# Optimization experiments

Hardware: AMD Instinct MI355X
Metric: run time of the kernel (lower is better)

The kernel has to match this reference:

```python
import jax, jax.numpy as jnp
import numpy as np

N, DEG, D_IN, D_HID = 50000, 16, 963, 256


def setup_inputs() -> dict:
    key = jax.random.key(0)
    ks = jax.random.split(key, 8)
    s = 0.02
    neighbours = jax.random.randint(ks[0], (N, DEG), 0, N)
    shape_features = jax.random.normal(ks[1], (N, D_IN), dtype=jnp.float32)
    # layer 0: D_IN -> D_HID; layers 1..13 (stacked): D_HID -> D_HID; extra: D_HID -> 3
    W_self0 = jax.random.normal(ks[2], (D_IN, D_HID), dtype=jnp.float32) * s
    W_neigh0 = jax.random.normal(ks[3], (D_IN, D_HID), dtype=jnp.float32) * s
    b0 = jnp.zeros((D_HID,), jnp.float32)
    W_self = jax.random.normal(ks[4], (13, D_HID, D_HID), dtype=jnp.float32) * s
    W_neigh = jax.random.normal(ks[5], (13, D_HID, D_HID), dtype=jnp.float32) * s
    b = jnp.zeros((13, D_HID), jnp.float32)
    W_extra = jax.random.normal(ks[6], (D_HID, 3), dtype=jnp.float32) * s
    b_extra = jnp.zeros((3,), jnp.float32)
    return {
        "neighbours": neighbours,
        "shape_features": shape_features,
        "W_self0": W_self0, "W_neigh0": W_neigh0, "b0": b0,
        "W_self": W_self, "W_neigh": W_neigh, "b": b,
        "W_extra": W_extra, "b_extra": b_extra,
    }


def _gcn(x, neighbours, Ws, Wn, bias):
    # gather neighbour features [N, DEG, D] and sum-aggregate, plus self transform
    agg = jnp.take(x, neighbours, axis=0).sum(axis=1)
    return x @ Ws + agg @ Wn + bias


def reference(neighbours, shape_features, W_self0, W_neigh0, b0, W_self, W_neigh, b, W_extra, b_extra):
    x = jax.nn.relu(_gcn(shape_features, neighbours, W_self0, W_neigh0, b0))
    for i in range(6):  # 6 residual blocks of 2 GCN layers each
        temp = x
        x = jax.nn.relu(_gcn(x, neighbours, W_self[2 * i], W_neigh[2 * i], b[2 * i]))
        x = jax.nn.relu(_gcn(x, neighbours, W_self[2 * i + 1], W_neigh[2 * i + 1], b[2 * i + 1]))
        x = (temp + x) / 2
    x = jax.nn.relu(_gcn(x, neighbours, W_self[12], W_neigh[12], b[12]))
    coordinates = x @ W_extra + b_extra  # extra layer called without neighbours -> linear
    return (x, coordinates)
```

## Files before the change

kernel.cpp:

```cpp
#include <hip/hip_runtime.h>
#include <hip/hip_bf16.h>
#include <hip/hip_fp16.h>
#include <stdint.h>

#define NNODES 50000
#define NPAD   50048
#define DEG    16
#define DIN    963
#define K0PAD  992
#define DHID   256
#define SCALE  (1.0f / 1024.0f)
#define ISCALE 1024.0f

typedef __attribute__((ext_vector_type(4))) float    f32x4;
typedef __attribute__((ext_vector_type(8))) _Float16 f16x8;
typedef __attribute__((ext_vector_type(4))) _Float16 f16x4;

typedef const __attribute__((address_space(1))) void GV;
typedef __attribute__((address_space(3))) void LV;

__device__ __forceinline__ void gl2lds16(const void* g, void* l) {
    __builtin_amdgcn_global_load_lds((GV*)g, (LV*)l, 16, 0, 0);
}

__global__ __launch_bounds__(256) void gemm_dual0(
    const _Float16* __restrict__ A, int K,
    const _Float16* __restrict__ Wp,
    _Float16* __restrict__ ys, _Float16* __restrict__ yn)
{
    __shared__ _Float16 lds[2][2][4096];

    const int tid  = threadIdx.x;
    const int w    = tid >> 6;
    const int lane = tid & 63;
    const int bm   = blockIdx.x * 128;
    const int nb   = blockIdx.y * 128;

    const int KT = K >> 5;

    auto stage = [&](int s, int kt) {
        const int k0 = kt << 5;
#pragma unroll
        for (int i = 0; i < 2; ++i) {
            const int j   = w + (i << 2);
            const int c   = (j << 6) + lane;
            const int row = c & 127;
            const int k8  = (c >> 7) << 3;
            gl2lds16(A  + (size_t)(bm + row) * K + k0 + k8, &lds[s][0][(size_t)j << 9]);
            gl2lds16(Wp + (size_t)(nb + row) * K + k0 + k8, &lds[s][1][(size_t)j << 9]);
        }
    };

    const int wm = (w >> 1) << 6;
    const int wn = (w & 1) << 6;
    const int lr = lane & 15;
    const int kh = lane >> 4;

    f32x4 acc[4][4] = {};

    stage(0, 0);
    __syncthreads();
    int cur = 0;
    for (int kt = 0; kt < KT; ++kt) {
        if (kt + 1 < KT) stage(cur ^ 1, kt + 1);
        f16x8 a[4], b[4];
#pragma unroll
        for (int mi = 0; mi < 4; ++mi)
            a[mi] = *(const f16x8*)&lds[cur][0][((kh << 7) + wm + (mi << 4) + lr) << 3];
#pragma unroll
        for (int ni = 0; ni < 4; ++ni)
            b[ni] = *(const f16x8*)&lds[cur][1][((kh << 7) + wn + (ni << 4) + lr) << 3];
#pragma unroll
        for (int mi = 0; mi < 4; ++mi)
#pragma unroll
            for (int ni = 0; ni < 4; ++ni)
                acc[mi][ni] = __builtin_amdgcn_mfma_f32_16x16x32_f16(a[mi], b[ni], acc[mi][ni], 0, 0, 0);
        __syncthreads();
        cur ^= 1;
    }

    _Float16* C = (blockIdx.y < 2) ? ys : yn;
    const int cb = (nb & 255) + wn;
#pragma unroll
    for (int mi = 0; mi < 4; ++mi) {
        const size_t rbase = (size_t)(bm + wm + (mi << 4) + (kh << 2)) << 8;
#pragma unroll
        for (int ni = 0; ni < 4; ++ni) {
            const int col = cb + (ni << 4) + lr;
#pragma unroll
            for (int r = 0; r < 4; ++r)
                C[rbase + ((size_t)r << 8) + col] = (_Float16)acc[mi][ni][r];
        }
    }
}

template<int FINAL>
__global__ __launch_bounds__(512) void fused_layer(
    const _Float16* __restrict__ X, const int* __restrict__ nbr,
    const _Float16* __restrict__ W, const float* __restrict__ bias,
    const _Float16* __restrict__ res,
    _Float16* __restrict__ outh, float* __restrict__ outf)
{
    __shared__ _Float16 ldsA[2][4096];
    __shared__ _Float16 ldsB[2][8192];

    const int tid  = threadIdx.x;
    const int w    = tid >> 6;
    const int lane = tid & 63;
    const int bm   = blockIdx.x << 7;

    const int growg = bm + (tid >> 2);
    const int nrow  = (growg < NNODES) ? growg : (NNODES - 1);
    const int4* np  = (const int4*)(nbr + nrow * DEG);
    const int4 q0 = np[0], q1 = np[1], q2 = np[2], q3 = np[3];
    const int kq = (tid & 3) << 3;

    auto stage = [&](int s, int kt) {
        if (kt < 8) {
            const int c = tid;
            gl2lds16(X + ((size_t)(bm + (c & 127)) << 8) + (kt << 5) + ((c >> 7) << 3),
                     &ldsA[s][(size_t)c << 3]);
        } else {
            const int kl = ((kt & 7) << 5) + kq;
            auto LD = [&](int r) -> f16x8 {
                return *(const f16x8*)(X + ((size_t)r << 8) + kl);
            };
            const f16x8 t0 = (LD(q0.x) + LD(q0.y)) + (LD(q0.z) + LD(q0.w));
            const f16x8 t1 = (LD(q1.x) + LD(q1.y)) + (LD(q1.z) + LD(q1.w));
            const f16x8 t2 = (LD(q2.x) + LD(q2.y)) + (LD(q2.z) + LD(q2.w));
            const f16x8 t3 = (LD(q3.x) + LD(q3.y)) + (LD(q3.z) + LD(q3.w));
            const f16x8 sum = (t0 + t1) + (t2 + t3);
            *(f16x8*)&ldsA[s][(size_t)(((tid & 3) << 7) + (tid >> 2)) << 3] = sum;
        }
#pragma unroll
        for (int i = 0; i < 2; ++i) {
            const int c = (i << 9) + tid;
            gl2lds16(W + ((size_t)(c & 255) << 9) + (kt << 5) + ((c >> 8) << 3),
                     &ldsB[s][(size_t)c << 3]);
        }
    };

    const int wm = (w >> 2) << 6;
    const int wn = (w & 3) << 6;
    const int lr = lane & 15;
    const int kh = lane >> 4;

    f32x4 acc[4][4] = {};

    stage(0, 0);
    __syncthreads();
    int cur = 0;
    for (int kt = 0; kt < 16; ++kt) {
        if (kt + 1 < 16) stage(cur ^ 1, kt + 1);
        f16x8 a[4], b[4];
#pragma unroll
        for (int mi = 0; mi < 4; ++mi)
            a[mi] = *(const f16x8*)&ldsA[cur][((kh << 7) + wm + (mi << 4) + lr) << 3];
#pragma unroll
        for (int ni = 0; ni < 4; ++ni)
            b[ni] = *(const f16x8*)&ldsB[cur][((kh << 8) + wn + (ni << 4) + lr) << 3];
#pragma unroll
        for (int mi = 0; mi < 4; ++mi)
#pragma unroll
            for (int ni = 0; ni < 4; ++ni)
                acc[mi][ni] = __builtin_amdgcn_mfma_f32_16x16x32_f16(a[mi], b[ni], acc[mi][ni], 0, 0, 0);
        __syncthreads();
        cur ^= 1;
    }

    const int r0 = kh << 2;
#pragma unroll
    for (int mi = 0; mi < 4; ++mi) {
        const int grow0 = bm + wm + (mi << 4) + r0;
#pragma unroll
        for (int ni = 0; ni < 4; ++ni) {
            const int col = wn + (ni << 4) + lr;
            const float bcol = bias[col] * SCALE;
#pragma unroll
            for (int r = 0; r < 4; ++r) {
                const int grow = grow0 + r;
                float s = acc[mi][ni][r] + bcol;
                s = fmaxf(s, 0.f);
                if (res) s = ((float)res[((size_t)grow << 8) + col] + s) * 0.5f;
                if (FINAL) {
                    if (grow < NNODES) outf[((size_t)grow << 8) + col] = s * ISCALE;
                } else {
                    outh[((size_t)grow << 8) + col] = (_Float16)s;
                }
            }
        }
    }
}

__global__ __launch_bounds__(256) void combine0(
    const _Float16* __restrict__ ys, const _Float16* __restrict__ yn,
    const int* __restrict__ nbr, const float* __restrict__ bias,
    _Float16* __restrict__ outh)
{
    const int w    = threadIdx.x >> 6;
    const int lane = threadIdx.x & 63;
    const int n    = (blockIdx.x << 2) + w;
    const int c4   = lane << 2;
    const size_t base = ((size_t)n << 8) + c4;

    const f16x4 ysv = *(const f16x4*)(ys + base);
    const float4 bv = *(const float4*)(bias + c4);
    float s0 = (float)ysv[0] + bv.x * SCALE;
    float s1 = (float)ysv[1] + bv.y * SCALE;
    float s2 = (float)ysv[2] + bv.z * SCALE;
    float s3 = (float)ysv[3] + bv.w * SCALE;

    const int* nr = nbr + n * DEG;
#pragma unroll
    for (int j = 0; j < DEG; ++j) {
        const f16x4 v = *(const f16x4*)(yn + (((size_t)nr[j]) << 8) + c4);
        s0 += (float)v[0]; s1 += (float)v[1]; s2 += (float)v[2]; s3 += (float)v[3];
    }
    f16x4 o;
    o[0] = (_Float16)fmaxf(s0, 0.f); o[1] = (_Float16)fmaxf(s1, 0.f);
    o[2] = (_Float16)fmaxf(s2, 0.f); o[3] = (_Float16)fmaxf(s3, 0.f);
    *(f16x4*)(outh + base) = o;
}

__global__ __launch_bounds__(64) void coords_kernel(
    const float* __restrict__ x, const float* __restrict__ We,
    const float* __restrict__ be, float* __restrict__ out3, int N)
{
    const int n = blockIdx.x;
    const int l = threadIdx.x;
    const float4 xv = *(const float4*)(x + (size_t)n * 256 + l * 4);
    float p0 = 0.f, p1 = 0.f, p2 = 0.f;
    const float xs[4] = {xv.x, xv.y, xv.z, xv.w};
#pragma unroll
    for (int i = 0; i < 4; ++i) {
        const int cidx = l * 4 + i;
        p0 += xs[i] * We[cidx * 3 + 0];
        p1 += xs[i] * We[cidx * 3 + 1];
        p2 += xs[i] * We[cidx * 3 + 2];
    }
#pragma unroll
    for (int off = 32; off > 0; off >>= 1) {
        p0 += __shfl_down(p0, off);
        p1 += __shfl_down(p1, off);
        p2 += __shfl_down(p2, off);
    }
    if (l == 0) {
        out3[(size_t)n * 3 + 0] = p0 + be[0];
        out3[(size_t)n * 3 + 1] = p1 + be[1];
        out3[(size_t)n * 3 + 2] = p2 + be[2];
    }
}

__global__ __launch_bounds__(256) void conv_sf(const float* __restrict__ sf,
                                               _Float16* __restrict__ sfb)
{
    const int idx = blockIdx.x * 256 + threadIdx.x;
    const int row = idx / 124;
    const int k8  = (idx % 124) << 3;
    f16x8 o = {};
    if (row < NNODES) {
#pragma unroll
        for (int i = 0; i < 8; ++i) {
            const int k = k8 + i;
            o[i] = (k < DIN) ? (_Float16)(sf[(size_t)row * DIN + k] * SCALE) : (_Float16)0.f;
        }
    }
    *(f16x8*)(sfb + (size_t)row * K0PAD + k8) = o;
}

__global__ __launch_bounds__(256) void pack_w0(const float* __restrict__ Ws0,
                                               const float* __restrict__ Wn0,
                                               _Float16* __restrict__ Wp0)
{
    const int idx = blockIdx.x * 256 + threadIdx.x;
    const int nn  = idx & 511;
    const int k8  = idx >> 9;
    const float* W = (nn < 256) ? Ws0 : Wn0;
    const int n0 = nn & 255;
    f16x8 o;
#pragma unroll
    for (int i = 0; i < 8; ++i) {
        const int k = (k8 << 3) + i;
        o[i] = (k < DIN) ? (_Float16)W[(size_t)k * 256 + n0] : (_Float16)0.f;
    }
    *(f16x8*)(Wp0 + (size_t)nn * K0PAD + (k8 << 3)) = o;
}

__global__ __launch_bounds__(256) void pack_w2(const float* __restrict__ Ws,
                                               const float* __restrict__ Wn,
                                               _Float16* __restrict__ Wpk2)
{
    const int idx = blockIdx.x * 256 + threadIdx.x;
    const int n   = idx & 255;
    const int k8  = (idx >> 8) & 63;
    const int l   = idx >> 14;
    f16x8 o;
#pragma unroll
    for (int i = 0; i < 8; ++i) {
        const int k = (k8 << 3) + i;
        const float* W = (k < 256) ? Ws : Wn;
        o[i] = (_Float16)W[(size_t)l * 65536 + (k & 255) * 256 + n];
    }
    *(f16x8*)(Wpk2 + (size_t)l * 131072 + (size_t)n * 512 + (k8 << 3)) = o;
}

extern "C" void kernel_launch(void* const* d_in, const int* in_sizes, int n_in,
                              void* d_out, int out_size, void* d_ws, size_t ws_size,
                              hipStream_t stream)
{
    const int*   nbr = (const int*)d_in[0];
    const float* sf  = (const float*)d_in[1];
    const float* Ws0 = (const float*)d_in[2];
    const float* Wn0 = (const float*)d_in[3];
    const float* b0  = (const float*)d_in[4];
    const float* Ws  = (const float*)d_in[5];
    const float* Wn  = (const float*)d_in[6];
    const float* bb  = (const float*)d_in[7];
    const float* We  = (const float*)d_in[8];
    const float* be  = (const float*)d_in[9];
    float* out = (float*)d_out;

    uint8_t* w = (uint8_t*)d_ws;
    _Float16* sfb  = (_Float16*)w;
    _Float16* P    = (_Float16*)w;
    _Float16* Q    = P + (size_t)NPAD * 256;
    _Float16* Wpk2 = Q + (size_t)NPAD * 256;
    _Float16* Wp0  = (_Float16*)(w + (size_t)NPAD * K0PAD * 2);
    _Float16* ysb  = Wp0 + (size_t)512 * K0PAD;
    _Float16* ynb  = ysb + (size_t)NPAD * 256;

    conv_sf<<<NPAD * 124 / 256, 256, 0, stream>>>(sf, sfb);
    pack_w0<<<512 * 124 / 256, 256, 0, stream>>>(Ws0, Wn0, Wp0);

    gemm_dual0<<<dim3(NPAD / 128, 4), 256, 0, stream>>>(sfb, K0PAD, Wp0, ysb, ynb);
    pack_w2<<<13 * 64 * 256 / 256, 256, 0, stream>>>(Ws, Wn, Wpk2);
    combine0<<<NNODES / 4, 256, 0, stream>>>(ysb, ynb, nbr, b0, P);

    const int fg = NPAD / 128;

    for (int t = 0; t < 6; ++t) {
        const int lA = 2 * t, lB = lA + 1;
        fused_layer<0><<<fg, 512, 0, stream>>>(P, nbr, Wpk2 + (size_t)lA * 131072,
                                               bb + lA * 256, nullptr, Q, nullptr);
        fused_layer<0><<<fg, 512, 0, stream>>>(Q, nbr, Wpk2 + (size_t)lB * 131072,
                                               bb + lB * 256, P, P, nullptr);
    }

    fused_layer<1><<<fg, 512, 0, stream>>>(P, nbr, Wpk2 + (size_t)12 * 131072,
                                           bb + 12 * 256, nullptr, nullptr, out);

    coords_kernel<<<NNODES, 64, 0, stream>>>(out, We, be, out + (size_t)NNODES * 256, NNODES);
}
```

Before: 1.591 ms.

## Restructure fused GCN layer: 64-row tiles, direct-global MFMA operands, pipelined gather

```diff
diff --git a/kernel.cpp b/kernel.cpp
--- a/kernel.cpp
+++ b/kernel.cpp
@@ -95,83 +95,102 @@
 }
 
 template<int FINAL>
-__global__ __launch_bounds__(512) void fused_layer(
+__global__ __launch_bounds__(256) void fused_layer(
     const _Float16* __restrict__ X, const int* __restrict__ nbr,
     const _Float16* __restrict__ W, const float* __restrict__ bias,
     const _Float16* __restrict__ res,
     _Float16* __restrict__ outh, float* __restrict__ outf)
 {
-    __shared__ _Float16 ldsA[2][4096];
-    __shared__ _Float16 ldsB[2][8192];
+    __shared__ _Float16 ldsG[2][2048];
 
     const int tid  = threadIdx.x;
     const int w    = tid >> 6;
     const int lane = tid & 63;
-    const int bm   = blockIdx.x << 7;
-
-    const int growg = bm + (tid >> 2);
+
+    const int nwg = gridDim.x, bid = blockIdx.x;
+    const int q = nwg >> 3, r_ = nwg & 7, xc = bid & 7;
+    const int wgid = (xc < r_ ? xc * (q + 1) : r_ * (q + 1) + (xc - r_) * q) + (bid >> 3);
+    const int bm = wgid << 6;
+
+    const int growg = bm + lane;
     const int nrow  = (growg < NNODES) ? growg : (NNODES - 1);
     const int4* np  = (const int4*)(nbr + nrow * DEG);
     const int4 q0 = np[0], q1 = np[1], q2 = np[2], q3 = np[3];
-    const int kq = (tid & 3) << 3;
-
-    auto stage = [&](int s, int kt) {
-        if (kt < 8) {
-            const int c = tid;
-            gl2lds16(X + ((size_t)(bm + (c & 127)) << 8) + (kt << 5) + ((c >> 7) << 3),
-                     &ldsA[s][(size_t)c << 3]);
-        } else {
-            const int kl = ((kt & 7) << 5) + kq;
-            auto LD = [&](int r) -> f16x8 {
-                return *(const f16x8*)(X + ((size_t)r << 8) + kl);
-            };
-            const f16x8 t0 = (LD(q0.x) + LD(q0.y)) + (LD(q0.z) + LD(q0.w));
-            const f16x8 t1 = (LD(q1.x) + LD(q1.y)) + (LD(q1.z) + LD(q1.w));
-            const f16x8 t2 = (LD(q2.x) + LD(q2.y)) + (LD(q2.z) + LD(q2.w));
-            const f16x8 t3 = (LD(q3.x) + LD(q3.y)) + (LD(q3.z) + LD(q3.w));
-            const f16x8 sum = (t0 + t1) + (t2 + t3);
-            *(f16x8*)&ldsA[s][(size_t)(((tid & 3) << 7) + (tid >> 2)) << 3] = sum;
-        }
-#pragma unroll
-        for (int i = 0; i < 2; ++i) {
-            const int c = (i << 9) + tid;
-            gl2lds16(W + ((size_t)(c & 255) << 9) + (kt << 5) + ((c >> 8) << 3),
-                     &ldsB[s][(size_t)c << 3]);
-        }
-    };
-
-    const int wm = (w >> 2) << 6;
-    const int wn = (w & 3) << 6;
+    const int kqo = w << 3;
+
+    const int wn = w << 6;
     const int lr = lane & 15;
     const int kh = lane >> 4;
 
     f32x4 acc[4][4] = {};
 
-    stage(0, 0);
-    __syncthreads();
-    int cur = 0;
-    for (int kt = 0; kt < 16; ++kt) {
-        if (kt + 1 < 16) stage(cur ^ 1, kt + 1);
+    auto GLD = [&](int r, int ko) -> f16x8 {
+        return *(const f16x8*)(X + ((size_t)r << 8) + ko);
+    };
+
+    f16x8 g0 = GLD(q0.x, kqo), g1 = GLD(q0.y, kqo), g2 = GLD(q0.z, kqo), g3 = GLD(q0.w, kqo);
+    f16x8 g4 = GLD(q1.x, kqo), g5 = GLD(q1.y, kqo), g6 = GLD(q1.z, kqo), g7 = GLD(q1.w, kqo);
+
+#pragma unroll
+    for (int kt = 0; kt < 8; ++kt) {
         f16x8 a[4], b[4];
 #pragma unroll
         for (int mi = 0; mi < 4; ++mi)
-            a[mi] = *(const f16x8*)&ldsA[cur][((kh << 7) + wm + (mi << 4) + lr) << 3];
+            a[mi] = *(const f16x8*)(X + ((size_t)(bm + (mi << 4) + lr) << 8) + (kt << 5) + (kh << 3));
 #pragma unroll
         for (int ni = 0; ni < 4; ++ni)
-            b[ni] = *(const f16x8*)&ldsB[cur][((kh << 8) + wn + (ni << 4) + lr) << 3];
+            b[ni] = *(const f16x8*)(W + ((size_t)(wn + (ni << 4) + lr) << 9) + (kt << 5) + (kh << 3));
 #pragma unroll
         for (int mi = 0; mi < 4; ++mi)
 #pragma unroll
             for (int ni = 0; ni < 4; ++ni)
                 acc[mi][ni] = __builtin_amdgcn_mfma_f32_16x16x32_f16(a[mi], b[ni], acc[mi][ni], 0, 0, 0);
+    }
+
+    {
+        f16x8 s0 = ((g0 + g1) + (g2 + g3)) + ((g4 + g5) + (g6 + g7));
+        g0 = GLD(q2.x, kqo); g1 = GLD(q2.y, kqo); g2 = GLD(q2.z, kqo); g3 = GLD(q2.w, kqo);
+        g4 = GLD(q3.x, kqo); g5 = GLD(q3.y, kqo); g6 = GLD(q3.z, kqo); g7 = GLD(q3.w, kqo);
+        f16x8 s1 = ((g0 + g1) + (g2 + g3)) + ((g4 + g5) + (g6 + g7));
+        *(f16x8*)&ldsG[0][(w << 9) + (lane << 3)] = s0 + s1;
+    }
+    __syncthreads();
+
+#pragma unroll
+    for (int kt = 8; kt < 16; ++kt) {
+        const int cb = kt & 1;
+        const int ko = ((kt - 7) << 5) + kqo;
+        f16x8 h0, h1, h2, h3, h4, h5, h6, h7;
+        if (kt < 15) {
+            h0 = GLD(q0.x, ko); h1 = GLD(q0.y, ko); h2 = GLD(q0.z, ko); h3 = GLD(q0.w, ko);
+            h4 = GLD(q1.x, ko); h5 = GLD(q1.y, ko); h6 = GLD(q1.z, ko); h7 = GLD(q1.w, ko);
+        }
+        f16x8 a[4], b[4];
+#pragma unroll
+        for (int ni = 0; ni < 4; ++ni)
+            b[ni] = *(const f16x8*)(W + ((size_t)(wn + (ni << 4) + lr) << 9) + (kt << 5) + (kh << 3));
+#pragma unroll
+        for (int mi = 0; mi < 4; ++mi)
+            a[mi] = *(const f16x8*)&ldsG[cb][(kh << 9) + (((mi << 4) + lr) << 3)];
+#pragma unroll
+        for (int mi = 0; mi < 4; ++mi)
+#pragma unroll
+            for (int ni = 0; ni < 4; ++ni)
+                acc[mi][ni] = __builtin_amdgcn_mfma_f32_16x16x32_f16(a[mi], b[ni], acc[mi][ni], 0, 0, 0);
+        if (kt < 15) {
+            f16x8 s0 = ((h0 + h1) + (h2 + h3)) + ((h4 + h5) + (h6 + h7));
+            h0 = GLD(q2.x, ko); h1 = GLD(q2.y, ko); h2 = GLD(q2.z, ko); h3 = GLD(q2.w, ko);
+            h4 = GLD(q3.x, ko); h5 = GLD(q3.y, ko); h6 = GLD(q3.z, ko); h7 = GLD(q3.w, ko);
+            f16x8 s1 = ((h0 + h1) + (h2 + h3)) + ((h4 + h5) + (h6 + h7));
+            *(f16x8*)&ldsG[cb ^ 1][(w << 9) + (lane << 3)] = s0 + s1;
+        }
         __syncthreads();
-        cur ^= 1;
     }
 
     const int r0 = kh << 2;
 #pragma unroll
     for (int mi = 0; mi < 4; ++mi) {
-        const int grow0 = bm + wm + (mi << 4) + r0;
+        const int grow0 = bm + (mi << 4) + r0;
 #pragma unroll
         for (int ni = 0; ni < 4; ++ni) {
             const int col = wn + (ni << 4) + lr;
@@ -336,17 +355,17 @@
     pack_w2<<<13 * 64 * 256 / 256, 256, 0, stream>>>(Ws, Wn, Wpk2);
     combine0<<<NNODES / 4, 256, 0, stream>>>(ysb, ynb, nbr, b0, P);
 
-    const int fg = NPAD / 128;
+    const int fg = NPAD / 64;
 
     for (int t = 0; t < 6; ++t) {
         const int lA = 2 * t, lB = lA + 1;
-        fused_layer<0><<<fg, 512, 0, stream>>>(P, nbr, Wpk2 + (size_t)lA * 131072,
+        fused_layer<0><<<fg, 256, 0, stream>>>(P, nbr, Wpk2 + (size_t)lA * 131072,
                                                bb + lA * 256, nullptr, Q, nullptr);
-        fused_layer<0><<<fg, 512, 0, stream>>>(Q, nbr, Wpk2 + (size_t)lB * 131072,
+        fused_layer<0><<<fg, 256, 0, stream>>>(Q, nbr, Wpk2 + (size_t)lB * 131072,
                                                bb + lB * 256, P, P, nullptr);
     }
 
-    fused_layer<1><<<fg, 512, 0, stream>>>(P, nbr, Wpk2 + (size_t)12 * 131072,
+    fused_layer<1><<<fg, 256, 0, stream>>>(P, nbr, Wpk2 + (size_t)12 * 131072,
                                            bb + 12 * 256, nullptr, nullptr, out);
 
     coords_kernel<<<NNODES, 64, 0, stream>>>(out, We, be, out + (size_t)NNODES * 256, NNODES);
```

After: 2.602 ms. 1.64x slower.

## Split fused gather+GEMM into separate gather kernel and N-tiled GEMM

Applied to the files above, without the earlier changes.

```diff
diff --git a/kernel.cpp b/kernel.cpp
--- a/kernel.cpp
+++ b/kernel.cpp
@@ -95,53 +95,37 @@
 }
 
 template<int FINAL>
-__global__ __launch_bounds__(512) void fused_layer(
-    const _Float16* __restrict__ X, const int* __restrict__ nbr,
-    const _Float16* __restrict__ W, const float* __restrict__ bias,
+__global__ __launch_bounds__(256) void gemm_hidden(
+    const _Float16* __restrict__ X, const _Float16* __restrict__ AG,
+    const _Float16* __restrict__ Wp,
+    const float* __restrict__ bias,
     const _Float16* __restrict__ res,
     _Float16* __restrict__ outh, float* __restrict__ outf)
 {
-    __shared__ _Float16 ldsA[2][4096];
-    __shared__ _Float16 ldsB[2][8192];
+    __shared__ _Float16 lds[2][2][4096];
 
     const int tid  = threadIdx.x;
     const int w    = tid >> 6;
     const int lane = tid & 63;
-    const int bm   = blockIdx.x << 7;
-
-    const int growg = bm + (tid >> 2);
-    const int nrow  = (growg < NNODES) ? growg : (NNODES - 1);
-    const int4* np  = (const int4*)(nbr + nrow * DEG);
-    const int4 q0 = np[0], q1 = np[1], q2 = np[2], q3 = np[3];
-    const int kq = (tid & 3) << 3;
+    const int bm   = blockIdx.x * 128;
+    const int nb   = blockIdx.y << 7;
 
     auto stage = [&](int s, int kt) {
-        if (kt < 8) {
-            const int c = tid;
-            gl2lds16(X + ((size_t)(bm + (c & 127)) << 8) + (kt << 5) + ((c >> 7) << 3),
-                     &ldsA[s][(size_t)c << 3]);
-        } else {
-            const int kl = ((kt & 7) << 5) + kq;
-            auto LD = [&](int r) -> f16x8 {
-                return *(const f16x8*)(X + ((size_t)r << 8) + kl);
-            };
-            const f16x8 t0 = (LD(q0.x) + LD(q0.y)) + (LD(q0.z) + LD(q0.w));
-            const f16x8 t1 = (LD(q1.x) + LD(q1.y)) + (LD(q1.z) + LD(q1.w));
-            const f16x8 t2 = (LD(q2.x) + LD(q2.y)) + (LD(q2.z) + LD(q2.w));
-            const f16x8 t3 = (LD(q3.x) + LD(q3.y)) + (LD(q3.z) + LD(q3.w));
-            const f16x8 sum = (t0 + t1) + (t2 + t3);
-            *(f16x8*)&ldsA[s][(size_t)(((tid & 3) << 7) + (tid >> 2)) << 3] = sum;
-        }
+        const _Float16* Asrc = (kt < 8) ? X : AG;
+        const int ka = (kt & 7) << 5;
 #pragma unroll
         for (int i = 0; i < 2; ++i) {
-            const int c = (i << 9) + tid;
-            gl2lds16(W + ((size_t)(c & 255) << 9) + (kt << 5) + ((c >> 8) << 3),
-                     &ldsB[s][(size_t)c << 3]);
+            const int j   = w + (i << 2);
+            const int c   = (j << 6) + lane;
+            const int row = c & 127;
+            const int k8  = (c >> 7) << 3;
+            gl2lds16(Asrc + ((size_t)(bm + row) << 8) + ka + k8, &lds[s][0][(size_t)j << 9]);
+            gl2lds16(Wp + (size_t)(nb + row) * 512 + (kt << 5) + k8, &lds[s][1][(size_t)j << 9]);
         }
     };
 
-    const int wm = (w >> 2) << 6;
-    const int wn = (w & 3) << 6;
+    const int wm = (w >> 1) << 6;
+    const int wn = (w & 1) << 6;
     const int lr = lane & 15;
     const int kh = lane >> 4;
 
@@ -155,10 +139,10 @@
         f16x8 a[4], b[4];
 #pragma unroll
         for (int mi = 0; mi < 4; ++mi)
-            a[mi] = *(const f16x8*)&ldsA[cur][((kh << 7) + wm + (mi << 4) + lr) << 3];
+            a[mi] = *(const f16x8*)&lds[cur][0][((kh << 7) + wm + (mi << 4) + lr) << 3];
 #pragma unroll
         for (int ni = 0; ni < 4; ++ni)
-            b[ni] = *(const f16x8*)&ldsB[cur][((kh << 8) + wn + (ni << 4) + lr) << 3];
+            b[ni] = *(const f16x8*)&lds[cur][1][((kh << 7) + wn + (ni << 4) + lr) << 3];
 #pragma unroll
         for (int mi = 0; mi < 4; ++mi)
 #pragma unroll
@@ -168,13 +152,12 @@
         cur ^= 1;
     }
 
-    const int r0 = kh << 2;
 #pragma unroll
     for (int mi = 0; mi < 4; ++mi) {
-        const int grow0 = bm + wm + (mi << 4) + r0;
+        const int grow0 = bm + wm + (mi << 4) + (kh << 2);
 #pragma unroll
         for (int ni = 0; ni < 4; ++ni) {
-            const int col = wn + (ni << 4) + lr;
+            const int col = nb + wn + (ni << 4) + lr;
             const float bcol = bias[col] * SCALE;
 #pragma unroll
             for (int r = 0; r < 4; ++r) {
@@ -192,34 +175,66 @@
     }
 }
 
-__global__ __launch_bounds__(256) void combine0(
+__global__ __launch_bounds__(256) void gather16(
+    const _Float16* __restrict__ X, const int* __restrict__ nbr,
+    _Float16* __restrict__ agg)
+{
+    const int idx = blockIdx.x * 256 + threadIdx.x;
+    const int r   = idx >> 5;
+    const int c8  = (idx & 31) << 3;
+    const int rr  = (r < NNODES) ? r : (NNODES - 1);
+    const int4* np = (const int4*)(nbr + rr * DEG);
+    const int4 q0 = np[0], q1 = np[1], q2 = np[2], q3 = np[3];
+
+    f16x8 v[16];
+#define LD16(slot, n) v[slot] = *(const f16x8*)(X + ((size_t)(n) << 8) + c8)
+    LD16(0,  q0.x); LD16(1,  q0.y); LD16(2,  q0.z); LD16(3,  q0.w);
+    LD16(4,  q1.x); LD16(5,  q1.y); LD16(6,  q1.z); LD16(7,  q1.w);
+    LD16(8,  q2.x); LD16(9,  q2.y); LD16(10, q2.z); LD16(11, q2.w);
+    LD16(12, q3.x); LD16(13, q3.y); LD16(14, q3.z); LD16(15, q3.w);
+#undef LD16
+    f16x8 o;
+#pragma unroll
+    for (int i = 0; i < 8; ++i) {
+        float s = 0.f;
+#pragma unroll
+        for (int j = 0; j < 16; ++j) s += (float)v[j][i];
+        o[i] = (_Float16)s;
+    }
+    *(f16x8*)(agg + ((size_t)r << 8) + c8) = o;
+}
+
+__global__ __launch_bounds__(256) void combine16(
     const _Float16* __restrict__ ys, const _Float16* __restrict__ yn,
     const int* __restrict__ nbr, const float* __restrict__ bias,
     _Float16* __restrict__ outh)
 {
-    const int w    = threadIdx.x >> 6;
-    const int lane = threadIdx.x & 63;
-    const int n    = (blockIdx.x << 2) + w;
-    const int c4   = lane << 2;
-    const size_t base = ((size_t)n << 8) + c4;
-
-    const f16x4 ysv = *(const f16x4*)(ys + base);
-    const float4 bv = *(const float4*)(bias + c4);
-    float s0 = (float)ysv[0] + bv.x * SCALE;
-    float s1 = (float)ysv[1] + bv.y * SCALE;
-    float s2 = (float)ysv[2] + bv.z * SCALE;
-    float s3 = (float)ysv[3] + bv.w * SCALE;
-
-    const int* nr = nbr + n * DEG;
-#pragma unroll
-    for (int j = 0; j < DEG; ++j) {
-        const f16x4 v = *(const f16x4*)(yn + (((size_t)nr[j]) << 8) + c4);
-        s0 += (float)v[0]; s1 += (float)v[1]; s2 += (float)v[2]; s3 += (float)v[3];
-    }
-    f16x4 o;
-    o[0] = (_Float16)fmaxf(s0, 0.f); o[1] = (_Float16)fmaxf(s1, 0.f);
-    o[2] = (_Float16)fmaxf(s2, 0.f); o[3] = (_Float16)fmaxf(s3, 0.f);
-    *(f16x4*)(outh + base) = o;
+    const int idx = blockIdx.x * 256 + threadIdx.x;
+    const int r   = idx >> 5;
+    const int c8  = (idx & 31) << 3;
+    const int4* np = (const int4*)(nbr + r * DEG);
+    const int4 q0 = np[0], q1 = np[1], q2 = np[2], q3 = np[3];
+
+    f16x8 v[16];
+#define LD16(slot, n) v[slot] = *(const f16x8*)(yn + ((size_t)(n) << 8) + c8)
+    LD16(0,  q0.x); LD16(1,  q0.y); LD16(2,  q0.z); LD16(3,  q0.w);
+    LD16(4,  q1.x); LD16(5,  q1.y); LD16(6,  q1.z); LD16(7,  q1.w);
+    LD16(8,  q2.x); LD16(9,  q2.y); LD16(10, q2.z); LD16(11, q2.w);
+    LD16(12, q3.x); LD16(13, q3.y); LD16(14, q3.z); LD16(15, q3.w);
+#undef LD16
+    const f16x8 ysv = *(const f16x8*)(ys + ((size_t)r << 8) + c8);
+    const float4 b0 = *(const float4*)(bias + c8);
+    const float4 b1 = *(const float4*)(bias + c8 + 4);
+    const float bb[8] = {b0.x, b0.y, b0.z, b0.w, b1.x, b1.y, b1.z, b1.w};
+    f16x8 o;
+#pragma unroll
+    for (int i = 0; i < 8; ++i) {
+        float s = (float)ysv[i] + bb[i] * SCALE;
+#pragma unroll
+        for (int j = 0; j < 16; ++j) s += (float)v[j][i];
+        o[i] = (_Float16)fmaxf(s, 0.f);
+    }
+    *(f16x8*)(outh + ((size_t)r << 8) + c8) = o;
 }
 
 __global__ __launch_bounds__(64) void coords_kernel(
@@ -324,29 +339,40 @@
     _Float16* sfb  = (_Float16*)w;
     _Float16* P    = (_Float16*)w;
     _Float16* Q    = P + (size_t)NPAD * 256;
-    _Float16* Wpk2 = Q + (size_t)NPAD * 256;
+    _Float16* R    = Q + (size_t)NPAD * 256;
+    _Float16* Wpk2 = R + (size_t)NPAD * 256;
     _Float16* Wp0  = (_Float16*)(w + (size_t)NPAD * K0PAD * 2);
     _Float16* ysb  = Wp0 + (size_t)512 * K0PAD;
     _Float16* ynb  = ysb + (size_t)NPAD * 256;
+    _Float16* agg  = ysb;
 
     conv_sf<<<NPAD * 124 / 256, 256, 0, stream>>>(sf, sfb);
     pack_w0<<<512 * 124 / 256, 256, 0, stream>>>(Ws0, Wn0, Wp0);
 
     gemm_dual0<<<dim3(NPAD / 128, 4), 256, 0, stream>>>(sfb, K0PAD, Wp0, ysb, ynb);
     pack_w2<<<13 * 64 * 256 / 256, 256, 0, stream>>>(Ws, Wn, Wpk2);
-    combine0<<<NNODES / 4, 256, 0, stream>>>(ysb, ynb, nbr, b0, P);
-
-    const int fg = NPAD / 128;
-
+    combine16<<<NNODES * 32 / 256, 256, 0, stream>>>(ysb, ynb, nbr, b0, P);
+
+    const dim3 hg(NPAD / 128, 2);
+    const int gg = NPAD * 32 / 256;
+
+    _Float16* buf[3] = {P, Q, R};
+    int xi = 0;
     for (int t = 0; t < 6; ++t) {
         const int lA = 2 * t, lB = lA + 1;
-        fused_layer<0><<<fg, 512, 0, stream>>>(P, nbr, Wpk2 + (size_t)lA * 131072,
-                                               bb + lA * 256, nullptr, Q, nullptr);
-        fused_layer<0><<<fg, 512, 0, stream>>>(Q, nbr, Wpk2 + (size_t)lB * 131072,
-                                               bb + lB * 256, P, P, nullptr);
-    }
-
-    fused_layer<1><<<fg, 512, 0, stream>>>(P, nbr, Wpk2 + (size_t)12 * 131072,
+        _Float16* a = buf[(xi + 1) % 3];
+        _Float16* b = buf[(xi + 2) % 3];
+        gather16<<<gg, 256, 0, stream>>>(buf[xi], nbr, agg);
+        gemm_hidden<0><<<hg, 256, 0, stream>>>(buf[xi], agg, Wpk2 + (size_t)lA * 131072,
+                                               bb + lA * 256, nullptr, a, nullptr);
+        gather16<<<gg, 256, 0, stream>>>(a, nbr, agg);
+        gemm_hidden<0><<<hg, 256, 0, stream>>>(a, agg, Wpk2 + (size_t)lB * 131072,
+                                               bb + lB * 256, buf[xi], b, nullptr);
+        xi = (xi + 2) % 3;
+    }
+
+    gather16<<<gg, 256, 0, stream>>>(buf[xi], nbr, agg);
+    gemm_hidden<1><<<hg, 256, 0, stream>>>(buf[xi], agg, Wpk2 + (size_t)12 * 131072,
                                            bb + 12 * 256, nullptr, nullptr, out);
 
     coords_kernel<<<NNODES, 64, 0, stream>>>(out, We, be, out + (size_t)NNODES * 256, NNODES);
```

Measured after the change: 1.742 ms. +9.5%, slower.
